# Optimization experiments

Hardware: AMD Instinct MI355X
Metric: run time of the kernel (lower is better)

The kernel has to match this reference:

```python
import jax, jax.numpy as jnp
import numpy as np

LN_EPS = 1e-3  # keras LayerNormalization default epsilon


def _layernorm(x, gamma, beta):
    mu = jnp.mean(x, axis=-1, keepdims=True)
    var = jnp.mean(jnp.square(x - mu), axis=-1, keepdims=True)
    return (x - mu) * jax.lax.rsqrt(var + LN_EPS) * gamma + beta


def setup_inputs() -> dict:
    key = jax.random.key(0)
    ks = jax.random.split(key, 8)
    B, H, W, C = 4, 64, 64, 256
    units = 256
    s = 1.0 / np.sqrt(C)  # he-normal-ish scale for 1x1 convs
    return {
        "inputs": jax.random.normal(ks[0], (B, H, W, C), jnp.float32),
        "context": jax.random.normal(ks[1], (B, H, W, C), jnp.float32),
        "Wq": jax.random.normal(ks[2], (C, units), jnp.float32) * s,
        "bq": jnp.zeros((units,), jnp.float32),
        "Wk": jax.random.normal(ks[3], (C, units), jnp.float32) * s,
        "bk": jnp.zeros((units,), jnp.float32),
        "Wv": jax.random.normal(ks[4], (C, units), jnp.float32) * s,
        "bv": jnp.zeros((units,), jnp.float32),
        "Wp": jax.random.normal(ks[5], (units, units), jnp.float32) * s,
        "bp": jnp.zeros((units,), jnp.float32),
        "gamma": jnp.ones((C,), jnp.float32),
        "beta": jnp.zeros((C,), jnp.float32),
    }


def reference(inputs, context, Wq, bq, Wk, bk, Wv, bv, Wp, bp, gamma, beta):
    B, H, W, C = inputs.shape
    units = Wq.shape[1]
    scale = jnp.float32(units) ** -0.5

    x_n = _layernorm(inputs, gamma, beta)          # normalized inputs (also residual base)
    q = jnp.einsum('bhwc,cu->bhwu', x_n, Wq) + bq   # [B,H,W,U]
    k = jnp.einsum('bhwc,cu->bhwu', context, Wk) + bk
    v = jnp.einsum('bhwc,cu->bhwu', context, Wv) + bv

    # full (h*w) x (H*W) score tensor, as in the original
    scores = jnp.einsum('bhwc,bHWc->bhwHW', q, k) * scale
    scores = scores.reshape(B, H, W, H * W)
    attn = jax.nn.softmax(scores, axis=-1).reshape(B, H, W, H, W)

    out = jnp.einsum('bhwHW,bHWc->bhwc', attn, v)
    proj = jnp.einsum('bhwc,cu->bhwu', out, Wp) + bp
    return x_n + proj
```

## Files before the change

kernel.cpp:

```cpp
#include <hip/hip_runtime.h>

typedef short v8s __attribute__((ext_vector_type(8)));
typedef float v4f __attribute__((ext_vector_type(4)));
using u16 = unsigned short;


__device__ __forceinline__ u16 f2b(float f) {
  union { float f; unsigned u; } v; v.f = f;
  unsigned r = v.u + 0x7FFFu + ((v.u >> 16) & 1u);
  return (u16)(r >> 16);
}

__global__ void ln_prep(const float* __restrict__ x, const float* __restrict__ ctx,
                        const float* __restrict__ gamma, const float* __restrict__ beta,
                        float* __restrict__ xn_f, u16* __restrict__ xn_b,
                        u16* __restrict__ ctx_b)
{
  const int tid = threadIdx.x;
  const int wid = tid >> 6, lane = tid & 63;
  const int row = blockIdx.x * 4 + wid;
  const size_t tidx = ((size_t)(row >> 4) * 8 + (lane >> 3)) * 512 +
                      (((lane >> 1) & 3) * 16 + (row & 15)) * 8 + (lane & 1) * 4;
  if (blockIdx.y == 0) {
    const float4 xv = *(const float4*)(x + (size_t)row * 256 + lane * 4);
    float s1 = xv.x + xv.y + xv.z + xv.w;
    float s2 = xv.x*xv.x + xv.y*xv.y + xv.z*xv.z + xv.w*xv.w;
#pragma unroll
    for (int m = 32; m >= 1; m >>= 1) {
      s1 += __shfl_xor(s1, m);
      s2 += __shfl_xor(s2, m);
    }
    const float mu  = s1 * (1.0f/256.0f);
    const float var = s2 * (1.0f/256.0f) - mu*mu;
    const float rs  = rsqrtf(var + 1e-3f);
    const float4 g = *(const float4*)(gamma + lane*4);
    const float4 b = *(const float4*)(beta  + lane*4);
    float4 y;
    y.x = (xv.x-mu)*rs*g.x + b.x;
    y.y = (xv.y-mu)*rs*g.y + b.y;
    y.z = (xv.z-mu)*rs*g.z + b.z;
    y.w = (xv.w-mu)*rs*g.w + b.w;
    *(float4*)(xn_f + (size_t)row*256 + lane*4) = y;
    ushort4 yb; yb.x=f2b(y.x); yb.y=f2b(y.y); yb.z=f2b(y.z); yb.w=f2b(y.w);
    *(ushort4*)(xn_b + tidx) = yb;
  } else {
    const float4 cv = *(const float4*)(ctx + (size_t)row * 256 + lane * 4);
    ushort4 cb; cb.x=f2b(cv.x); cb.y=f2b(cv.y); cb.z=f2b(cv.z); cb.w=f2b(cv.w);
    *(ushort4*)(ctx_b + tidx) = cb;
  }
}

__global__ void wtrans(const float* __restrict__ wq, const float* __restrict__ wk,
                       const float* __restrict__ wv, const float* __restrict__ wp,
                       u16* __restrict__ tq, u16* __restrict__ tk,
                       u16* __restrict__ tv, u16* __restrict__ tp)
{
  const float* src; u16* dst;
  switch (blockIdx.y) {
    case 0:  src = wq; dst = tq; break;
    case 1:  src = wk; dst = tk; break;
    case 2:  src = wv; dst = tv; break;
    default: src = wp; dst = tp; break;
  }
  const int t  = threadIdx.x;
  const int kk = blockIdx.x * 16 + (t >> 4);
  const int n0 = (t & 15) * 16;
  const size_t base = (size_t)((t & 15) * 8 + (kk >> 5)) * 512 +
                      ((kk >> 3) & 3) * 16 * 8 + (kk & 7);
#pragma unroll
  for (int j = 0; j < 16; j++)
    dst[base + (size_t)j * 8] = f2b(src[(size_t)kk * 256 + n0 + j]);
}

__global__ __launch_bounds__(256) void gemm_qkv(
    const u16* __restrict__ xn_b, const u16* __restrict__ ctx_b,
    const u16* __restrict__ wqt, const u16* __restrict__ wkt, const u16* __restrict__ wvt,
    const float* __restrict__ bq, const float* __restrict__ bk, const float* __restrict__ bv,
    u16* __restrict__ qo, u16* __restrict__ ko, u16* __restrict__ vto)
{
  const int mode = blockIdx.y;
  const u16* A; const u16* Wt; const float* bias;
  if (mode == 0)      { A = xn_b;  Wt = wqt; bias = bq; }
  else if (mode == 1) { A = ctx_b; Wt = wkt; bias = bk; }
  else                { A = ctx_b; Wt = wvt; bias = bv; }
  const int wid = threadIdx.x >> 6, lane = threadIdx.x & 63;
  const int lm = lane & 15, q4 = lane >> 4;
  const int m0 = blockIdx.x * 64 + wid * 16;
  const u16* abase = A + (size_t)(m0 >> 4) * 4096 + lane * 8;
  v8s af[8];
#pragma unroll
  for (int kf = 0; kf < 8; kf++) af[kf] = *(const v8s*)(abase + kf * 512);
#pragma unroll
  for (int ct = 0; ct < 16; ct++) {
    const int c = ct * 16 + lm;
    const u16* wbase = Wt + (size_t)ct * 4096 + lane * 8;
    v4f acc = {0.f, 0.f, 0.f, 0.f};
#pragma unroll
    for (int kf = 0; kf < 8; kf++)
      acc = __builtin_amdgcn_mfma_f32_16x16x32_bf16(af[kf], *(const v8s*)(wbase + kf * 512), acc, 0, 0, 0);
    const float bb = bias[c];
    if (mode == 2) {
      const int b = m0 >> 12;
      const int chunk = (m0 & 4095) >> 6;
      const int kic = (m0 & 63) + q4 * 4;
      const int ks = kic >> 5;
      const int q4p = (kic >> 3) & 3;
      const size_t idx = ((size_t)(b * 64 + chunk) * 32 + (c >> 4) * 2 + ks) * 512 +
                         (q4p * 16 + (c & 15)) * 8 + (q4 & 1) * 4;
      ushort4 pk;
      pk.x = f2b(acc[0] + bb); pk.y = f2b(acc[1] + bb);
      pk.z = f2b(acc[2] + bb); pk.w = f2b(acc[3] + bb);
      *(ushort4*)(vto + idx) = pk;
    } else {
      u16* out = (mode == 0) ? qo : ko;
      const size_t base = ((size_t)(m0 >> 4) * 8 + (c >> 5)) * 512 +
                          (((c >> 3) & 3) * 16 + q4 * 4) * 8 + (c & 7);
#pragma unroll
      for (int r = 0; r < 4; r++)
        out[base + (size_t)r * 8] = f2b(acc[r] + bb);
    }
  }
}

__global__ __launch_bounds__(256, 1) void attn_kernel(
    const u16* __restrict__ q, const u16* __restrict__ k,
    const u16* __restrict__ vt, u16* __restrict__ ao)
{
  __shared__ u16 P[2][64][72];
  __shared__ float Lp[4][64];
  __shared__ float Lt[64];
  const int b   = blockIdx.y;
  const int tid = threadIdx.x;
  const int w   = tid >> 6, lane = tid & 63;
  const int lm  = lane & 15, q4 = lane >> 4;
  const int m0  = blockIdx.x * 64;
  const u16* qb = q  + (size_t)b * 1048576;
  const u16* kb = k  + (size_t)b * 1048576;
  const u16* vb = vt + (size_t)b * 1048576;

  v8s qf[4][8];
#pragma unroll
  for (int qt = 0; qt < 4; qt++) {
    const u16* qbase = qb + (size_t)((m0 >> 4) + qt) * 4096 + lane * 8;
#pragma unroll
    for (int kf = 0; kf < 8; kf++) qf[qt][kf] = *(const v8s*)(qbase + kf * 512);
  }

  v4f o[4][4];
#pragma unroll
  for (int qt = 0; qt < 4; qt++)
#pragma unroll
    for (int ct = 0; ct < 4; ct++) o[qt][ct] = (v4f){0.f, 0.f, 0.f, 0.f};
  float lsum[4] = {0.f, 0.f, 0.f, 0.f};

  v8s kfr[8];
  {
    const u16* kbase = kb + (size_t)(w) * 4096 + lane * 8;
#pragma unroll
    for (int kf = 0; kf < 8; kf++) kfr[kf] = *(const v8s*)(kbase + kf * 512);
  }

  for (int s0 = 0; s0 < 4096; s0 += 64) {
    const int pb = (s0 >> 6) & 1;
    const int chunk = s0 >> 6;
    v8s vfr[4][2];
#pragma unroll
    for (int ct = 0; ct < 4; ct++) {
      const u16* vbase = vb + ((size_t)chunk * 32 + (w * 4 + ct) * 2) * 512 + lane * 8;
      vfr[ct][0] = *(const v8s*)(vbase);
      vfr[ct][1] = *(const v8s*)(vbase + 512);
    }
    v4f sc[4];
#pragma unroll
    for (int qt = 0; qt < 4; qt++) sc[qt] = (v4f){0.f, 0.f, 0.f, 0.f};
#pragma unroll
    for (int kf = 0; kf < 8; kf++)
#pragma unroll
      for (int qt = 0; qt < 4; qt++)
        sc[qt] = __builtin_amdgcn_mfma_f32_16x16x32_bf16(kfr[kf], qf[qt][kf], sc[qt], 0, 0, 0);
    {
      const int sn = (s0 + 64) & 4095;
      const u16* kbase = kb + (size_t)((sn >> 4) + w) * 4096 + lane * 8;
#pragma unroll
      for (int kf = 0; kf < 8; kf++) kfr[kf] = *(const v8s*)(kbase + kf * 512);
    }
#pragma unroll
    for (int qt = 0; qt < 4; qt++) {
      const float e0 = exp2f(sc[qt][0] * 0.09016844f);
      const float e1 = exp2f(sc[qt][1] * 0.09016844f);
      const float e2 = exp2f(sc[qt][2] * 0.09016844f);
      const float e3 = exp2f(sc[qt][3] * 0.09016844f);
      lsum[qt] += (e0 + e1) + (e2 + e3);
      unsigned d0, d1;
      asm("v_cvt_pk_bf16_f32 %0, %1, %2" : "=v"(d0) : "v"(e0), "v"(e1));
      asm("v_cvt_pk_bf16_f32 %0, %1, %2" : "=v"(d1) : "v"(e2), "v"(e3));
      uint2 pk; pk.x = d0; pk.y = d1;
      *(uint2*)(&P[pb][qt * 16 + lm][w * 16 + q4 * 4]) = pk;
    }
    __syncthreads();
#pragma unroll
    for (int qt = 0; qt < 4; qt++) {
      const v8s pf0 = *(const v8s*)(&P[pb][qt * 16 + lm][q4 * 8]);
      const v8s pf1 = *(const v8s*)(&P[pb][qt * 16 + lm][32 + q4 * 8]);
#pragma unroll
      for (int ct = 0; ct < 4; ct++) {
        o[qt][ct] = __builtin_amdgcn_mfma_f32_16x16x32_bf16(pf0, vfr[ct][0], o[qt][ct], 0, 0, 0);
        o[qt][ct] = __builtin_amdgcn_mfma_f32_16x16x32_bf16(pf1, vfr[ct][1], o[qt][ct], 0, 0, 0);
      }
    }
  }

#pragma unroll
  for (int qt = 0; qt < 4; qt++) {
    float t = lsum[qt];
    t += __shfl_xor(t, 16);
    t += __shfl_xor(t, 32);
    lsum[qt] = t;
  }
  if (q4 == 0) {
#pragma unroll
    for (int qt = 0; qt < 4; qt++) Lp[w][qt * 16 + lm] = lsum[qt];
  }
  __syncthreads();
  if (tid < 64) Lt[tid] = Lp[0][tid] + Lp[1][tid] + Lp[2][tid] + Lp[3][tid];
  __syncthreads();

  const int rstrip0 = (b * 4096 + m0) >> 4;
#pragma unroll
  for (int qt = 0; qt < 4; qt++)
#pragma unroll
    for (int r = 0; r < 4; r++) {
      const float linv = 1.0f / Lt[qt * 16 + q4 * 4 + r];
#pragma unroll
      for (int ct = 0; ct < 4; ct++) {
        const int ch = w * 64 + ct * 16 + lm;
        const size_t idx = ((size_t)(rstrip0 + qt) * 8 + (ch >> 5)) * 512 +
                           (((ch >> 3) & 3) * 16 + q4 * 4 + r) * 8 + (ch & 7);
        ao[idx] = f2b(o[qt][ct][r] * linv);
      }
    }
}

__global__ __launch_bounds__(256) void gemm_proj(
    const u16* __restrict__ A, const u16* __restrict__ Wt, const float* __restrict__ bias,
    const float* __restrict__ xn_f, float* __restrict__ out)
{
  const int wid = threadIdx.x >> 6, lane = threadIdx.x & 63;
  const int lm = lane & 15, q4 = lane >> 4;
  const int m0 = blockIdx.x * 64 + wid * 16;
  const u16* abase = A + (size_t)(m0 >> 4) * 4096 + lane * 8;
  v8s af[8];
#pragma unroll
  for (int kf = 0; kf < 8; kf++) af[kf] = *(const v8s*)(abase + kf * 512);
#pragma unroll
  for (int ct = 0; ct < 16; ct++) {
    const int c = ct * 16 + lm;
    const u16* wbase = Wt + (size_t)ct * 4096 + lane * 8;
    v4f acc = {0.f, 0.f, 0.f, 0.f};
#pragma unroll
    for (int kf = 0; kf < 8; kf++)
      acc = __builtin_amdgcn_mfma_f32_16x16x32_bf16(af[kf], *(const v8s*)(wbase + kf * 512), acc, 0, 0, 0);
    const float bb = bias[c];
#pragma unroll
    for (int r = 0; r < 4; r++) {
      const size_t idx = (size_t)(m0 + q4 * 4 + r) * 256 + c;
      out[idx] = xn_f[idx] + acc[r] + bb;
    }
  }
}

extern "C" void kernel_launch(void* const* d_in, const int* in_sizes, int n_in,
                              void* d_out, int out_size, void* d_ws, size_t ws_size,
                              hipStream_t stream)
{
  (void)in_sizes; (void)n_in; (void)out_size; (void)ws_size;
  const float* inputs  = (const float*)d_in[0];
  const float* context = (const float*)d_in[1];
  const float* Wq = (const float*)d_in[2];
  const float* bq = (const float*)d_in[3];
  const float* Wk = (const float*)d_in[4];
  const float* bk = (const float*)d_in[5];
  const float* Wv = (const float*)d_in[6];
  const float* bv = (const float*)d_in[7];
  const float* Wp = (const float*)d_in[8];
  const float* bp = (const float*)d_in[9];
  const float* gamma = (const float*)d_in[10];
  const float* beta  = (const float*)d_in[11];
  float* out = (float*)d_out;

  char* p = (char*)d_ws;
  float* xn_f = (float*)p; p += (size_t)16384 * 256 * 4;
  u16* xn_b   = (u16*)p;   p += (size_t)16384 * 256 * 2;
  u16* ctx_b  = (u16*)p;   p += (size_t)16384 * 256 * 2;
  u16* qbuf   = (u16*)p;   p += (size_t)16384 * 256 * 2;
  u16* kbuf   = (u16*)p;   p += (size_t)16384 * 256 * 2;
  u16* vtbuf  = (u16*)p;   p += (size_t)16384 * 256 * 2;
  u16* wqt = (u16*)p; p += (size_t)256 * 256 * 2;
  u16* wkt = (u16*)p; p += (size_t)256 * 256 * 2;
  u16* wvt = (u16*)p; p += (size_t)256 * 256 * 2;
  u16* wpt = (u16*)p; p += (size_t)256 * 256 * 2;
  u16* aobuf = xn_b;

  ln_prep<<<dim3(4096, 2), 256, 0, stream>>>(inputs, context, gamma, beta, xn_f, xn_b, ctx_b);
  wtrans<<<dim3(16, 4), 256, 0, stream>>>(Wq, Wk, Wv, Wp, wqt, wkt, wvt, wpt);
  gemm_qkv<<<dim3(256, 3), 256, 0, stream>>>(xn_b, ctx_b, wqt, wkt, wvt, bq, bk, bv, qbuf, kbuf, vtbuf);
  attn_kernel<<<dim3(64, 4), 256, 0, stream>>>(qbuf, kbuf, vtbuf, aobuf);
  gemm_proj<<<dim3(256), 256, 0, stream>>>(aobuf, wpt, bp, xn_f, out);
}
```

Measured before the change: 248.3 us.

## Halve attention query tile to 32 rows, fold softmax scale into Wq, split GEMM accumulators

The attention kernel now processes 32 query rows per block instead of 64 and launches 512 blocks in a 1D grid with a batch-interleaved mapping, allowing two blocks per CU. This raises parallelism on a 256-CU part that previously had only 256 blocks. The softmax scale (including log2e) is folded into Wq and bq during weight prep, which removes a multiply per score. The QKV and projection GEMMs preload weight fragments and use four independent accumulators to break the MFMA dependency chain. The cost is that K/V are streamed twice as often per query row, and rounding Wq to bf16 after scaling changes precision slightly.

```diff
diff --git a/kernel.cpp b/kernel.cpp
--- a/kernel.cpp
+++ b/kernel.cpp
@@ -4,6 +4,7 @@
 typedef float v4f __attribute__((ext_vector_type(4)));
 using u16 = unsigned short;
 
+#define QSCALE 0.09016844f
 
 __device__ __forceinline__ u16 f2b(float f) {
   union { float f; unsigned u; } v; v.f = f;
@@ -55,9 +56,9 @@
                        u16* __restrict__ tq, u16* __restrict__ tk,
                        u16* __restrict__ tv, u16* __restrict__ tp)
 {
-  const float* src; u16* dst;
+  const float* src; u16* dst; float scl = 1.0f;
   switch (blockIdx.y) {
-    case 0:  src = wq; dst = tq; break;
+    case 0:  src = wq; dst = tq; scl = QSCALE; break;
     case 1:  src = wk; dst = tk; break;
     case 2:  src = wv; dst = tv; break;
     default: src = wp; dst = tp; break;
@@ -69,7 +70,7 @@
                       ((kk >> 3) & 3) * 16 * 8 + (kk & 7);
 #pragma unroll
   for (int j = 0; j < 16; j++)
-    dst[base + (size_t)j * 8] = f2b(src[(size_t)kk * 256 + n0 + j]);
+    dst[base + (size_t)j * 8] = f2b(src[(size_t)kk * 256 + n0 + j] * scl);
 }
 
 __global__ __launch_bounds__(256) void gemm_qkv(
@@ -83,6 +84,7 @@
   if (mode == 0)      { A = xn_b;  Wt = wqt; bias = bq; }
   else if (mode == 1) { A = ctx_b; Wt = wkt; bias = bk; }
   else                { A = ctx_b; Wt = wvt; bias = bv; }
+  const float bscale = (mode == 0) ? QSCALE : 1.0f;
   const int wid = threadIdx.x >> 6, lane = threadIdx.x & 63;
   const int lm = lane & 15, q4 = lane >> 4;
   const int m0 = blockIdx.x * 64 + wid * 16;
@@ -94,11 +96,20 @@
   for (int ct = 0; ct < 16; ct++) {
     const int c = ct * 16 + lm;
     const u16* wbase = Wt + (size_t)ct * 4096 + lane * 8;
-    v4f acc = {0.f, 0.f, 0.f, 0.f};
-#pragma unroll
-    for (int kf = 0; kf < 8; kf++)
-      acc = __builtin_amdgcn_mfma_f32_16x16x32_bf16(af[kf], *(const v8s*)(wbase + kf * 512), acc, 0, 0, 0);
-    const float bb = bias[c];
+    v8s wf[8];
+#pragma unroll
+    for (int kf = 0; kf < 8; kf++) wf[kf] = *(const v8s*)(wbase + kf * 512);
+    v4f a0 = {0.f,0.f,0.f,0.f}, a1 = a0, a2 = a0, a3 = a0;
+    a0 = __builtin_amdgcn_mfma_f32_16x16x32_bf16(af[0], wf[0], a0, 0, 0, 0);
+    a1 = __builtin_amdgcn_mfma_f32_16x16x32_bf16(af[2], wf[2], a1, 0, 0, 0);
+    a2 = __builtin_amdgcn_mfma_f32_16x16x32_bf16(af[4], wf[4], a2, 0, 0, 0);
+    a3 = __builtin_amdgcn_mfma_f32_16x16x32_bf16(af[6], wf[6], a3, 0, 0, 0);
+    a0 = __builtin_amdgcn_mfma_f32_16x16x32_bf16(af[1], wf[1], a0, 0, 0, 0);
+    a1 = __builtin_amdgcn_mfma_f32_16x16x32_bf16(af[3], wf[3], a1, 0, 0, 0);
+    a2 = __builtin_amdgcn_mfma_f32_16x16x32_bf16(af[5], wf[5], a2, 0, 0, 0);
+    a3 = __builtin_amdgcn_mfma_f32_16x16x32_bf16(af[7], wf[7], a3, 0, 0, 0);
+    const v4f acc = (a0 + a1) + (a2 + a3);
+    const float bb = bias[c] * bscale;
     if (mode == 2) {
       const int b = m0 >> 12;
       const int chunk = (m0 & 4095) >> 6;
@@ -122,40 +133,42 @@
   }
 }
 
-__global__ __launch_bounds__(256, 1) void attn_kernel(
+__global__ __launch_bounds__(256, 2) void attn_kernel(
     const u16* __restrict__ q, const u16* __restrict__ k,
     const u16* __restrict__ vt, u16* __restrict__ ao)
 {
-  __shared__ u16 P[2][64][72];
-  __shared__ float Lp[4][64];
-  __shared__ float Lt[64];
-  const int b   = blockIdx.y;
+  __shared__ u16 P[2][32][72];
+  __shared__ float Lp[4][32];
+  __shared__ float Lt[32];
+  const int bid  = blockIdx.x;
+  const int b    = (bid & 7) >> 1;
+  const int qblk = ((bid >> 3) << 1) | (bid & 1);
   const int tid = threadIdx.x;
   const int w   = tid >> 6, lane = tid & 63;
   const int lm  = lane & 15, q4 = lane >> 4;
-  const int m0  = blockIdx.x * 64;
+  const int m0  = qblk * 32;
   const u16* qb = q  + (size_t)b * 1048576;
   const u16* kb = k  + (size_t)b * 1048576;
   const u16* vb = vt + (size_t)b * 1048576;
 
-  v8s qf[4][8];
-#pragma unroll
-  for (int qt = 0; qt < 4; qt++) {
+  v8s qf[2][8];
+#pragma unroll
+  for (int qt = 0; qt < 2; qt++) {
     const u16* qbase = qb + (size_t)((m0 >> 4) + qt) * 4096 + lane * 8;
 #pragma unroll
     for (int kf = 0; kf < 8; kf++) qf[qt][kf] = *(const v8s*)(qbase + kf * 512);
   }
 
-  v4f o[4][4];
-#pragma unroll
-  for (int qt = 0; qt < 4; qt++)
+  v4f o[2][4];
+#pragma unroll
+  for (int qt = 0; qt < 2; qt++)
 #pragma unroll
     for (int ct = 0; ct < 4; ct++) o[qt][ct] = (v4f){0.f, 0.f, 0.f, 0.f};
-  float lsum[4] = {0.f, 0.f, 0.f, 0.f};
+  float lsum[2] = {0.f, 0.f};
 
   v8s kfr[8];
   {
-    const u16* kbase = kb + (size_t)(w) * 4096 + lane * 8;
+    const u16* kbase = kb + (size_t)w * 4096 + lane * 8;
 #pragma unroll
     for (int kf = 0; kf < 8; kf++) kfr[kf] = *(const v8s*)(kbase + kf * 512);
   }
@@ -170,13 +183,13 @@
       vfr[ct][0] = *(const v8s*)(vbase);
       vfr[ct][1] = *(const v8s*)(vbase + 512);
     }
-    v4f sc[4];
-#pragma unroll
-    for (int qt = 0; qt < 4; qt++) sc[qt] = (v4f){0.f, 0.f, 0.f, 0.f};
+    v4f sc[2];
+#pragma unroll
+    for (int qt = 0; qt < 2; qt++) sc[qt] = (v4f){0.f, 0.f, 0.f, 0.f};
 #pragma unroll
     for (int kf = 0; kf < 8; kf++)
 #pragma unroll
-      for (int qt = 0; qt < 4; qt++)
+      for (int qt = 0; qt < 2; qt++)
         sc[qt] = __builtin_amdgcn_mfma_f32_16x16x32_bf16(kfr[kf], qf[qt][kf], sc[qt], 0, 0, 0);
     {
       const int sn = (s0 + 64) & 4095;
@@ -185,11 +198,11 @@
       for (int kf = 0; kf < 8; kf++) kfr[kf] = *(const v8s*)(kbase + kf * 512);
     }
 #pragma unroll
-    for (int qt = 0; qt < 4; qt++) {
-      const float e0 = exp2f(sc[qt][0] * 0.09016844f);
-      const float e1 = exp2f(sc[qt][1] * 0.09016844f);
-      const float e2 = exp2f(sc[qt][2] * 0.09016844f);
-      const float e3 = exp2f(sc[qt][3] * 0.09016844f);
+    for (int qt = 0; qt < 2; qt++) {
+      const float e0 = exp2f(sc[qt][0]);
+      const float e1 = exp2f(sc[qt][1]);
+      const float e2 = exp2f(sc[qt][2]);
+      const float e3 = exp2f(sc[qt][3]);
       lsum[qt] += (e0 + e1) + (e2 + e3);
       unsigned d0, d1;
       asm("v_cvt_pk_bf16_f32 %0, %1, %2" : "=v"(d0) : "v"(e0), "v"(e1));
@@ -199,7 +212,7 @@
     }
     __syncthreads();
 #pragma unroll
-    for (int qt = 0; qt < 4; qt++) {
+    for (int qt = 0; qt < 2; qt++) {
       const v8s pf0 = *(const v8s*)(&P[pb][qt * 16 + lm][q4 * 8]);
       const v8s pf1 = *(const v8s*)(&P[pb][qt * 16 + lm][32 + q4 * 8]);
 #pragma unroll
@@ -211,7 +224,7 @@
   }
 
 #pragma unroll
-  for (int qt = 0; qt < 4; qt++) {
+  for (int qt = 0; qt < 2; qt++) {
     float t = lsum[qt];
     t += __shfl_xor(t, 16);
     t += __shfl_xor(t, 32);
@@ -219,15 +232,15 @@
   }
   if (q4 == 0) {
 #pragma unroll
-    for (int qt = 0; qt < 4; qt++) Lp[w][qt * 16 + lm] = lsum[qt];
+    for (int qt = 0; qt < 2; qt++) Lp[w][qt * 16 + lm] = lsum[qt];
   }
   __syncthreads();
-  if (tid < 64) Lt[tid] = Lp[0][tid] + Lp[1][tid] + Lp[2][tid] + Lp[3][tid];
+  if (tid < 32) Lt[tid] = Lp[0][tid] + Lp[1][tid] + Lp[2][tid] + Lp[3][tid];
   __syncthreads();
 
   const int rstrip0 = (b * 4096 + m0) >> 4;
 #pragma unroll
-  for (int qt = 0; qt < 4; qt++)
+  for (int qt = 0; qt < 2; qt++)
 #pragma unroll
     for (int r = 0; r < 4; r++) {
       const float linv = 1.0f / Lt[qt * 16 + q4 * 4 + r];
@@ -256,10 +269,19 @@
   for (int ct = 0; ct < 16; ct++) {
     const int c = ct * 16 + lm;
     const u16* wbase = Wt + (size_t)ct * 4096 + lane * 8;
-    v4f acc = {0.f, 0.f, 0.f, 0.f};
-#pragma unroll
-    for (int kf = 0; kf < 8; kf++)
-      acc = __builtin_amdgcn_mfma_f32_16x16x32_bf16(af[kf], *(const v8s*)(wbase + kf * 512), acc, 0, 0, 0);
+    v8s wf[8];
+#pragma unroll
+    for (int kf = 0; kf < 8; kf++) wf[kf] = *(const v8s*)(wbase + kf * 512);
+    v4f a0 = {0.f,0.f,0.f,0.f}, a1 = a0, a2 = a0, a3 = a0;
+    a0 = __builtin_amdgcn_mfma_f32_16x16x32_bf16(af[0], wf[0], a0, 0, 0, 0);
+    a1 = __builtin_amdgcn_mfma_f32_16x16x32_bf16(af[2], wf[2], a1, 0, 0, 0);
+    a2 = __builtin_amdgcn_mfma_f32_16x16x32_bf16(af[4], wf[4], a2, 0, 0, 0);
+    a3 = __builtin_amdgcn_mfma_f32_16x16x32_bf16(af[6], wf[6], a3, 0, 0, 0);
+    a0 = __builtin_amdgcn_mfma_f32_16x16x32_bf16(af[1], wf[1], a0, 0, 0, 0);
+    a1 = __builtin_amdgcn_mfma_f32_16x16x32_bf16(af[3], wf[3], a1, 0, 0, 0);
+    a2 = __builtin_amdgcn_mfma_f32_16x16x32_bf16(af[5], wf[5], a2, 0, 0, 0);
+    a3 = __builtin_amdgcn_mfma_f32_16x16x32_bf16(af[7], wf[7], a3, 0, 0, 0);
+    const v4f acc = (a0 + a1) + (a2 + a3);
     const float bb = bias[c];
 #pragma unroll
     for (int r = 0; r < 4; r++) {
@@ -304,6 +326,6 @@
   ln_prep<<<dim3(4096, 2), 256, 0, stream>>>(inputs, context, gamma, beta, xn_f, xn_b, ctx_b);
   wtrans<<<dim3(16, 4), 256, 0, stream>>>(Wq, Wk, Wv, Wp, wqt, wkt, wvt, wpt);
   gemm_qkv<<<dim3(256, 3), 256, 0, stream>>>(xn_b, ctx_b, wqt, wkt, wvt, bq, bk, bv, qbuf, kbuf, vtbuf);
-  attn_kernel<<<dim3(64, 4), 256, 0, stream>>>(qbuf, kbuf, vtbuf, aobuf);
+  attn_kernel<<<dim3(512), 256, 0, stream>>>(qbuf, kbuf, vtbuf, aobuf);
   gemm_proj<<<dim3(256), 256, 0, stream>>>(aobuf, wpt, bp, xn_f, out);
 }
```

Result: faster. 224.7 us (-9.5%).
